# Optimization experiments

Hardware: AMD Instinct MI355X
Metric: run time of the kernel (lower is better)

## Reference

```python
import jax, jax.numpy as jnp
import numpy as np

B, T, C = 2, 2048, 2048
N_HEAD, N_KV_HEAD = 16, 4
HEAD_DIM = C // N_HEAD  # 128
N_REP = N_HEAD // N_KV_HEAD  # 4


def setup_inputs() -> dict:
    key = jax.random.key(0)
    ks = jax.random.split(key, 5)
    x = jax.random.normal(ks[0], (B, T, C), dtype=jnp.float32)
    # RoPE freqs (theta=10000), real cos/sin form of torch's complex freqs_cis
    inv_freq = 1.0 / (10000.0 ** (jnp.arange(0, HEAD_DIM, 2, dtype=jnp.float32) / HEAD_DIM))
    angles = jnp.arange(T, dtype=jnp.float32)[:, None] * inv_freq[None, :]  # [T, HEAD_DIM//2]
    freqs_cos = jnp.cos(angles)
    freqs_sin = jnp.sin(angles)
    s = 0.02
    wq = jax.random.normal(ks[1], (C, C), dtype=jnp.float32) * s
    wk = jax.random.normal(ks[2], (N_KV_HEAD * HEAD_DIM, C), dtype=jnp.float32) * s
    wv = jax.random.normal(ks[3], (N_KV_HEAD * HEAD_DIM, C), dtype=jnp.float32) * s
    wo = jax.random.normal(ks[4], (C, C), dtype=jnp.float32) * s
    return {"x": x, "freqs_cos": freqs_cos, "freqs_sin": freqs_sin,
            "wq": wq, "wk": wk, "wv": wv, "wo": wo}


def _apply_rotary(t, cos, sin):
    # t: [B, T, H, D]; pairs (even, odd) treated as complex, multiplied by cos+i*sin
    tr = t.reshape(*t.shape[:-1], -1, 2)  # [B,T,H,D/2,2]
    t0, t1 = tr[..., 0], tr[..., 1]
    c = cos[None, :, None, :]  # [1,T,1,D/2]
    s = sin[None, :, None, :]
    out = jnp.stack([t0 * c - t1 * s, t0 * s + t1 * c], axis=-1)
    return out.reshape(t.shape)


def reference(x, freqs_cos, freqs_sin, wq, wk, wv, wo):
    b, t, _ = x.shape
    xq = (x @ wq.T).reshape(b, t, N_HEAD, HEAD_DIM)
    xk = (x @ wk.T).reshape(b, t, N_KV_HEAD, HEAD_DIM)
    xv = (x @ wv.T).reshape(b, t, N_KV_HEAD, HEAD_DIM)
    xq = _apply_rotary(xq, freqs_cos, freqs_sin)
    xk = _apply_rotary(xk, freqs_cos, freqs_sin)
    # GQA: repeat_interleave kv heads to n_head
    xk_r = jnp.repeat(xk, N_REP, axis=2)
    xv_r = jnp.repeat(xv, N_REP, axis=2)
    # [B,H,T,D]
    q = xq.transpose(0, 2, 1, 3)
    k = xk_r.transpose(0, 2, 1, 3)
    v = xv_r.transpose(0, 2, 1, 3)
    scale = 1.0 / jnp.sqrt(jnp.float32(HEAD_DIM))
    scores = jnp.einsum('bhtd,bhsd->bhts', q, k) * scale
    causal = jnp.tril(jnp.ones((t, t), dtype=bool))
    scores = jnp.where(causal[None, None], scores, jnp.finfo(scores.dtype).min)
    attn = jax.nn.softmax(scores, axis=-1)
    y = jnp.einsum('bhts,bhsd->bhtd', attn, v)
    y = y.transpose(0, 2, 1, 3).reshape(b, t, C)
    return y @ wo.T
```

## Files before the change

### kernel.cpp

```cpp
#include <hip/hip_runtime.h>

typedef __attribute__((ext_vector_type(8))) __bf16 bf16x8;
typedef __attribute__((ext_vector_type(4))) __bf16 bf16x4;
typedef __attribute__((ext_vector_type(4))) float floatx4;

#define MFMA16x16x32 __builtin_amdgcn_mfma_f32_16x16x32_bf16

__device__ __forceinline__ void async_load16(const void* g, void* l) {
  __builtin_amdgcn_global_load_lds((const __attribute__((address_space(1))) void*)g,
                                   (__attribute__((address_space(3))) void*)l, 16, 0, 0);
}

__global__ __launch_bounds__(256) void cast_all_kernel(const float* __restrict__ x,
                                                       const float* __restrict__ wq,
                                                       const float* __restrict__ wk,
                                                       const float* __restrict__ wv,
                                                       const float* __restrict__ wo,
                                                       __bf16* __restrict__ dst) {
  int i = blockIdx.x * blockDim.x + threadIdx.x;
  const float* src;
  int off;
  if (i < 2097152)      { src = x;  off = 0; }
  else if (i < 3145728) { src = wq; off = 2097152; }
  else if (i < 3407872) { src = wk; off = 3145728; }
  else if (i < 3670016) { src = wv; off = 3407872; }
  else                  { src = wo; off = 3670016; }
  float4 v = ((const float4*)src)[i - off];
  bf16x4 o;
  o[0] = (__bf16)v.x; o[1] = (__bf16)v.y; o[2] = (__bf16)v.z; o[3] = (__bf16)v.w;
  *(bf16x4*)(dst + (size_t)i * 4) = o;
}

template <int MODE>
__global__ __launch_bounds__(256, 3) void gemm_bt(const __bf16* __restrict__ A,
                                                  const __bf16* __restrict__ Bw,
                                                  float* __restrict__ C,
                                                  const float* __restrict__ cs,
                                                  const float* __restrict__ sn,
                                                  __bf16* __restrict__ qb,
                                                  __bf16* __restrict__ kb,
                                                  __bf16* __restrict__ vtg,
                                                  int M, int N, int K) {
  __shared__ __bf16 As[128][64];
  __shared__ __bf16 Bs[128][64];
  const int tid = threadIdx.x;
  const int wave = tid >> 6, lane = tid & 63;
  const int quad = lane >> 4, l16 = lane & 15;
  const int wm = (wave >> 1) * 64, wn = (wave & 1) * 64;
  const int row0 = blockIdx.y * 128, col0 = blockIdx.x * 128;
  const int lr = lane >> 3, ls = lane & 7;
  const int segg = ls ^ lr;
  floatx4 acc[4][4] = {};
  const __bf16* Ab = A + (size_t)row0 * K + segg * 8;
  const __bf16* Bb = Bw + (size_t)col0 * K + segg * 8;
  for (int k0 = 0; k0 < K; k0 += 64) {
    __syncthreads();
#pragma unroll
    for (int i = 0; i < 4; i++) {
      int c = wave * 4 + i;
      int r = c * 8 + lr;
      async_load16(Ab + (size_t)r * K + k0, &As[c * 8][0]);
      async_load16(Bb + (size_t)r * K + k0, &Bs[c * 8][0]);
    }
    __syncthreads();
#pragma unroll
    for (int kk = 0; kk < 64; kk += 32) {
      bf16x8 af[4], bfr[4];
#pragma unroll
      for (int mt = 0; mt < 4; mt++) {
        int row = wm + mt * 16 + l16;
        int seg = ((kk >> 3) + quad) ^ (row & 7);
        af[mt] = *(const bf16x8*)&As[row][seg * 8];
      }
#pragma unroll
      for (int nt = 0; nt < 4; nt++) {
        int row = wn + nt * 16 + l16;
        int seg = ((kk >> 3) + quad) ^ (row & 7);
        bfr[nt] = *(const bf16x8*)&Bs[row][seg * 8];
      }
#pragma unroll
      for (int mt = 0; mt < 4; mt++)
#pragma unroll
        for (int nt = 0; nt < 4; nt++)
          acc[mt][nt] = MFMA16x16x32(af[mt], bfr[nt], acc[mt][nt], 0, 0, 0);
    }
  }
  if (MODE == 0) {
#pragma unroll
    for (int mt = 0; mt < 4; mt++)
#pragma unroll
      for (int nt = 0; nt < 4; nt++)
#pragma unroll
        for (int r = 0; r < 4; r++) {
          int row = row0 + wm + mt * 16 + quad * 4 + r;
          int col = col0 + wn + nt * 16 + l16;
          C[(size_t)row * N + col] = acc[mt][nt][r];
        }
  } else {
#pragma unroll
    for (int mt = 0; mt < 4; mt++)
#pragma unroll
      for (int nt = 0; nt < 4; nt++) {
        const int cbase = col0 + wn + nt * 16;
        if (cbase < 2560) {
          const int c = cbase + l16;
#pragma unroll
          for (int r = 0; r < 4; r++) {
            int row = row0 + wm + mt * 16 + quad * 4 + r;
            int t = row & 2047;
            float v = acc[mt][nt][r];
            float vp = __shfl_xor(v, 1);
            int i = (c & 127) >> 1;
            float co = cs[t * 64 + i], si = sn[t * 64 + i];
            float rv = v * co + ((c & 1) ? vp : -vp) * si;
            if (cbase < 2048) {
              qb[(size_t)row * 2048 + c] = (__bf16)(rv * 0.1275411391f);
            } else {
              kb[(size_t)row * 512 + c - 2048] = (__bf16)rv;
            }
          }
        }
      }
    __syncthreads();
    __bf16* Vl = &As[0][0] + wave * 1024;
    const int brow = row0 + wm;
#pragma unroll
    for (int nt = 0; nt < 4; nt++) {
      const int cbase = col0 + wn + nt * 16;
      if (cbase >= 2560) {
#pragma unroll
        for (int mt = 0; mt < 4; mt++)
#pragma unroll
          for (int r = 0; r < 4; r++)
            Vl[l16 * 64 + mt * 16 + quad * 4 + r] = (__bf16)acc[mt][nt][r];
        asm volatile("" ::: "memory");
        const int vB = cbase - 2560;
#pragma unroll
        for (int p = 0; p < 4; p++) {
          int vdl = p * 4 + (lane >> 4);
          int tl = (lane & 15) * 4;
          bf16x4 val = *(const bf16x4*)&Vl[vdl * 64 + tl];
          *(bf16x4*)&vtg[((size_t)(brow >> 11) * 512 + vB + vdl) * 2048 +
                         (brow & 2047) + tl] = val;
        }
        asm volatile("" ::: "memory");
      }
    }
  }
}

__global__ __launch_bounds__(256, 2) void attn_kernel(const __bf16* __restrict__ qb,
                                                      const __bf16* __restrict__ kb,
                                                      const __bf16* __restrict__ vtg,
                                                      __bf16* __restrict__ yb) {
  const int id = blockIdx.x;
  const int q1 = id >> 8;
  const int cc = id & 255;
  const int kvh = cc & 3;
  const int b = (cc >> 2) & 1;
  const int s5 = (cc >> 3) & 31;
  const int tile = q1 ? (63 - s5) : s5;
  const int tid = threadIdx.x, wave = tid >> 6, lane = tid & 63;
  const int h = kvh * 4 + wave;
  const int quad = lane >> 4, l16 = lane & 15;
  const int q0 = tile * 32;
  __shared__ __bf16 Ks[2][64][128];
  __shared__ __bf16 Vt[2][128][64];
  __shared__ __bf16 Ps[4][2][16][64];
  const __bf16* kbase = kb + (size_t)b * 2048 * 512 + kvh * 128;
  const __bf16* vbase = vtg + ((size_t)b * 512 + kvh * 128) * 2048;

  const int u16   = (quad ^ (l16 & 3)) * 16;
  const int b2_64 = (l16 & 4) ? 64 : 0;
  char* const ksb = (char*)Ks;
  char* const vtb = (char*)Vt;
  char* const psb = (char*)Ps + wave * 4096;
  char* const kA0 = ksb + l16 * 256 + u16 + b2_64;
  char* const kB0 = kA0 + 64 - 2 * b2_64;
  char* const kA1 = kA0 + 16384;
  char* const kB1 = kB0 + 16384;
  char* const vA0 = vtb + l16 * 128 + u16 + b2_64;
  char* const vB0 = vA0 + 64 - 2 * b2_64;
  char* const vA1 = vA0 + 16384;
  char* const vB1 = vB0 + 16384;
  char* const prA = psb + l16 * 128 + u16 + b2_64;
  char* const prB = prA + 64 - 2 * b2_64;
  const int h16 = (l16 & 8) ? 16 : 0;
  const int q64 = (quad & 1) * 64;
  char* const pw00 = psb + quad * 512 + (l16 & 7) * 2 + h16 + q64;
  char* const pw10 = psb + quad * 512 + (l16 & 7) * 2 + (16 - h16) + q64;
  char* const pw01 = pw00 + 64 - 2 * q64;
  char* const pw11 = pw10 + 64 - 2 * q64;

  const int klr4 = lane >> 4, kls = lane & 15;
  const int vlr8 = lane >> 3, vls = lane & 7;
  const __bf16* ksrc[4];
  const __bf16* vsrc[4];
#pragma unroll
  for (int i = 0; i < 4; i++) {
    int row = (wave * 4 + i) * 4 + klr4;
    ksrc[i] = kbase + (size_t)row * 512 + (kls ^ (row & 7)) * 8;
    int d = (wave * 4 + i) * 8 + vlr8;
    vsrc[i] = vbase + (size_t)d * 2048 + (vls ^ (d & 7)) * 8;
  }
  char* const kdst = ksb + wave * 4096;
  char* const vdst = vtb + wave * 4096;

  auto stage = [&](int pb, int s0) {
#pragma unroll
    for (int i = 0; i < 4; i++)
      async_load16(ksrc[i] + (size_t)s0 * 512, kdst + pb * 16384 + i * 1024);
#pragma unroll
    for (int i = 0; i < 4; i++)
      async_load16(vsrc[i] + s0, vdst + pb * 16384 + i * 1024);
  };

  bf16x8 qf[2][4];
#pragma unroll
  for (int mt = 0; mt < 2; mt++)
#pragma unroll
    for (int kc = 0; kc < 4; kc++)
      qf[mt][kc] = *(const bf16x8*)(qb + (size_t)(b * 2048 + q0 + mt * 16 + l16) * 2048 +
                                    h * 128 + kc * 32 + quad * 8);
  bf16x8 ones;
#pragma unroll
  for (int j = 0; j < 8; j++) ones[j] = (__bf16)1.0f;
  floatx4 o[2][8] = {};
  floatx4 lsum[2] = {};
  const int nblocks = (tile + 2) >> 1;

  stage(0, 0);

  for (int it = 0; it < nblocks; it++) {
    const int cur = it & 1;
    const int s0 = it * 64;
    asm volatile("s_barrier" ::: "memory");
    if (it + 1 < nblocks) {
      stage(cur ^ 1, s0 + 64);
      asm volatile("s_waitcnt vmcnt(8)" ::: "memory");
    } else {
      asm volatile("s_waitcnt vmcnt(0)" ::: "memory");
    }
    asm volatile("s_barrier" ::: "memory");
    const char* kA = cur ? kA1 : kA0;
    const char* kB = cur ? kB1 : kB0;
    const char* vA = cur ? vA1 : vA0;
    const char* vB = cur ? vB1 : vB0;
    floatx4 sacc[2][4] = {};
    __builtin_amdgcn_s_setprio(1);
#pragma unroll
    for (int kc = 0; kc < 4; kc++) {
      const char* kbp = (kc & 1) ? kB : kA;
      bf16x8 bfr[4];
#pragma unroll
      for (int nt = 0; nt < 4; nt++)
        bfr[nt] = *(const bf16x8*)(kbp + nt * 4096 + (kc >> 1) * 128);
#pragma unroll
      for (int mt = 0; mt < 2; mt++)
#pragma unroll
        for (int nt = 0; nt < 4; nt++)
          sacc[mt][nt] = MFMA16x16x32(qf[mt][kc], bfr[nt], sacc[mt][nt], 0, 0, 0);
    }
    __builtin_amdgcn_s_setprio(0);
    const bool diag = (it == nblocks - 1);
#pragma unroll
    for (int mt = 0; mt < 2; mt++)
#pragma unroll
      for (int r = 0; r < 4; r++) {
        const int qg = q0 + mt * 16 + quad * 4 + r;
#pragma unroll
        for (int nt = 0; nt < 4; nt++) {
          float p = __builtin_exp2f(sacc[mt][nt][r]);
          if (diag) { int keyg = s0 + nt * 16 + l16; p = (keyg <= qg) ? p : 0.f; }
          char* w = (r & 1) ? ((nt < 2) ? pw10 : pw11) : ((nt < 2) ? pw00 : pw01);
          *(__bf16*)(w + mt * 2048 + r * 128 + ((nt & 1) ^ (r >> 1)) * 32) = (__bf16)p;
        }
      }
    __builtin_amdgcn_s_setprio(1);
#pragma unroll
    for (int c2 = 0; c2 < 2; c2++) {
      const char* pr = c2 ? prB : prA;
      const char* vv = c2 ? vB : vA;
      bf16x8 pa[2];
#pragma unroll
      for (int mt = 0; mt < 2; mt++) {
        pa[mt] = *(const bf16x8*)(pr + mt * 2048);
        lsum[mt] = MFMA16x16x32(pa[mt], ones, lsum[mt], 0, 0, 0);
      }
#pragma unroll
      for (int dt = 0; dt < 8; dt++) {
        bf16x8 vf = *(const bf16x8*)(vv + dt * 2048);
#pragma unroll
        for (int mt = 0; mt < 2; mt++)
          o[mt][dt] = MFMA16x16x32(pa[mt], vf, o[mt][dt], 0, 0, 0);
      }
    }
    __builtin_amdgcn_s_setprio(0);
  }
#pragma unroll
  for (int mt = 0; mt < 2; mt++) {
    float inv[4];
#pragma unroll
    for (int r = 0; r < 4; r++) inv[r] = 1.f / lsum[mt][r];
#pragma unroll
    for (int dt = 0; dt < 8; dt++)
#pragma unroll
      for (int r = 0; r < 4; r++) {
        int qg = q0 + mt * 16 + quad * 4 + r;
        yb[(size_t)(b * 2048 + qg) * 2048 + h * 128 + dt * 16 + l16] =
            (__bf16)(o[mt][dt][r] * inv[r]);
      }
  }
}

extern "C" void kernel_launch(void* const* d_in, const int* in_sizes, int n_in,
                              void* d_out, int out_size, void* d_ws, size_t ws_size,
                              hipStream_t stream) {
  const float* x  = (const float*)d_in[0];
  const float* fc = (const float*)d_in[1];
  const float* fs = (const float*)d_in[2];
  const float* wq = (const float*)d_in[3];
  const float* wk = (const float*)d_in[4];
  const float* wv = (const float*)d_in[5];
  const float* wo = (const float*)d_in[6];
  float* out = (float*)d_out;
  char* ws = (char*)d_ws;

  __bf16* xb   = (__bf16*)(ws);
  __bf16* wqkv = (__bf16*)(ws + 16777216);
  __bf16* wob  = (__bf16*)(ws + 29360128);
  __bf16* qbuf = (__bf16*)(ws + 37748736);
  __bf16* kbuf = (__bf16*)(ws + 54525952);
  __bf16* vtg  = (__bf16*)(ws + 58720256);
  __bf16* ybuf = (__bf16*)(ws + 62914560);

  cast_all_kernel<<<18432, 256, 0, stream>>>(x, wq, wk, wv, wo, xb);

  gemm_bt<1><<<dim3(24, 32), 256, 0, stream>>>(xb, wqkv, nullptr, fc, fs,
                                               qbuf, kbuf, vtg, 4096, 3072, 2048);

  attn_kernel<<<dim3(512), 256, 0, stream>>>(qbuf, kbuf, vtg, ybuf);

  gemm_bt<0><<<dim3(16, 32), 256, 0, stream>>>(ybuf, wob, out, nullptr, nullptr,
                                               nullptr, nullptr, nullptr, 4096, 2048, 2048);
}
```

Baseline: 307.6 us.

## Split attention key range across two wave groups with LDS reduction

```diff
diff --git a/kernel.cpp b/kernel.cpp
--- a/kernel.cpp
+++ b/kernel.cpp
@@ -149,167 +149,194 @@
   }
 }
 
-__global__ __launch_bounds__(256, 2) void attn_kernel(const __bf16* __restrict__ qb,
+__global__ __launch_bounds__(512, 4) void attn_kernel(const __bf16* __restrict__ qb,
                                                       const __bf16* __restrict__ kb,
                                                       const __bf16* __restrict__ vtg,
                                                       __bf16* __restrict__ yb) {
   const int id = blockIdx.x;
-  const int q1 = id >> 8;
-  const int cc = id & 255;
-  const int kvh = cc & 3;
-  const int b = (cc >> 2) & 1;
-  const int s5 = (cc >> 3) & 31;
-  const int tile = q1 ? (63 - s5) : s5;
+  const int kvh = id & 3, b = (id >> 2) & 1;
+  const int tile = id >> 3;
   const int tid = threadIdx.x, wave = tid >> 6, lane = tid & 63;
-  const int h = kvh * 4 + wave;
+  const int ck = wave >> 2, hw = wave & 3;
+  const int h = kvh * 4 + hw;
   const int quad = lane >> 4, l16 = lane & 15;
   const int q0 = tile * 32;
-  __shared__ __bf16 Ks[2][64][128];
+  const int nk = tile + 1;
+  const int c0 = nk >> 1;
+  const int L = nk - c0;
+
+  __shared__ __bf16 Ks[2][2][32][128];
   __shared__ __bf16 Vt[2][128][64];
-  __shared__ __bf16 Ps[4][2][16][64];
+  __shared__ __bf16 Ps[8][2][16][32];
+
   const __bf16* kbase = kb + (size_t)b * 2048 * 512 + kvh * 128;
   const __bf16* vbase = vtg + ((size_t)b * 512 + kvh * 128) * 2048;
 
-  const int u16   = (quad ^ (l16 & 3)) * 16;
+  const int kl = lane >> 4, ks16 = lane & 15;
+  const __bf16* ksrc[2]; char* kdst[2];
+#pragma unroll
+  for (int jj = 0; jj < 2; jj++) {
+    int krow = hw * 8 + jj * 4 + kl;
+    ksrc[jj] = kbase + (size_t)krow * 512 + (ks16 ^ (krow & 7)) * 8;
+    kdst[jj] = (char*)Ks + ck * 8192 + (hw * 8 + jj * 4) * 256;
+  }
+  const int vdl = lane >> 2, vks = lane & 3;
+  const __bf16* vsrc[2]; char* vdst[2];
+#pragma unroll
+  for (int jj = 0; jj < 2; jj++) {
+    int d = hw * 32 + jj * 16 + vdl;
+    vsrc[jj] = vbase + (size_t)d * 2048 + vks * 8;
+    vdst[jj] = (char*)Vt + d * 128 + (((ck * 4 + vks) ^ (d & 7)) * 16);
+  }
+
+  const int u16 = (quad ^ (l16 & 3)) * 16;
   const int b2_64 = (l16 & 4) ? 64 : 0;
-  char* const ksb = (char*)Ks;
-  char* const vtb = (char*)Vt;
-  char* const psb = (char*)Ps + wave * 4096;
-  char* const kA0 = ksb + l16 * 256 + u16 + b2_64;
+  char* const kA0 = (char*)Ks + ck * 8192 + l16 * 256 + u16 + b2_64;
   char* const kB0 = kA0 + 64 - 2 * b2_64;
-  char* const kA1 = kA0 + 16384;
-  char* const kB1 = kB0 + 16384;
-  char* const vA0 = vtb + l16 * 128 + u16 + b2_64;
-  char* const vB0 = vA0 + 64 - 2 * b2_64;
-  char* const vA1 = vA0 + 16384;
-  char* const vB1 = vB0 + 16384;
-  char* const prA = psb + l16 * 128 + u16 + b2_64;
-  char* const prB = prA + 64 - 2 * b2_64;
-  const int h16 = (l16 & 8) ? 16 : 0;
-  const int q64 = (quad & 1) * 64;
-  char* const pw00 = psb + quad * 512 + (l16 & 7) * 2 + h16 + q64;
-  char* const pw10 = psb + quad * 512 + (l16 & 7) * 2 + (16 - h16) + q64;
-  char* const pw01 = pw00 + 64 - 2 * q64;
-  char* const pw11 = pw10 + 64 - 2 * q64;
-
-  const int klr4 = lane >> 4, kls = lane & 15;
-  const int vlr8 = lane >> 3, vls = lane & 7;
-  const __bf16* ksrc[4];
-  const __bf16* vsrc[4];
-#pragma unroll
-  for (int i = 0; i < 4; i++) {
-    int row = (wave * 4 + i) * 4 + klr4;
-    ksrc[i] = kbase + (size_t)row * 512 + (kls ^ (row & 7)) * 8;
-    int d = (wave * 4 + i) * 8 + vlr8;
-    vsrc[i] = vbase + (size_t)d * 2048 + (vls ^ (d & 7)) * 8;
-  }
-  char* const kdst = ksb + wave * 4096;
-  char* const vdst = vtb + wave * 4096;
-
-  auto stage = [&](int pb, int s0) {
-#pragma unroll
-    for (int i = 0; i < 4; i++)
-      async_load16(ksrc[i] + (size_t)s0 * 512, kdst + pb * 16384 + i * 1024);
-#pragma unroll
-    for (int i = 0; i < 4; i++)
-      async_load16(vsrc[i] + s0, vdst + pb * 16384 + i * 1024);
-  };
-
-  bf16x8 qf[2][4];
-#pragma unroll
-  for (int mt = 0; mt < 2; mt++)
-#pragma unroll
-    for (int kc = 0; kc < 4; kc++)
-      qf[mt][kc] = *(const bf16x8*)(qb + (size_t)(b * 2048 + q0 + mt * 16 + l16) * 2048 +
-                                    h * 128 + kc * 32 + quad * 8);
+  char* const vrd0 = (char*)Vt + l16 * 128 + u16 + ((ck ^ ((l16 >> 2) & 1)) ? 64 : 0);
+  char* const psb = (char*)Ps + wave * 2048;
+  char* const prd = psb + l16 * 64 + u16;
+  const int h3 = (l16 >> 3) & 1;
+  char* const pwE = psb + quad * 256 + (l16 & 7) * 2 + h3 * 16;
+  char* const pwO = psb + quad * 256 + (l16 & 7) * 2 + 16 - h3 * 16;
+
   bf16x8 ones;
 #pragma unroll
   for (int j = 0; j < 8; j++) ones[j] = (__bf16)1.0f;
   floatx4 o[2][8] = {};
   floatx4 lsum[2] = {};
-  const int nblocks = (tile + 2) >> 1;
-
-  stage(0, 0);
-
-  for (int it = 0; it < nblocks; it++) {
-    const int cur = it & 1;
-    const int s0 = it * 64;
+
+  {
+    const int g0 = ck ? c0 : 0;
+    bf16x8 v0 = *(const bf16x8*)(vsrc[0] + g0 * 32);
+    bf16x8 v1 = *(const bf16x8*)(vsrc[1] + g0 * 32);
+#pragma unroll
+    for (int jj = 0; jj < 2; jj++)
+      async_load16(ksrc[jj] + (size_t)g0 * 16384, kdst[jj]);
+    *(bf16x8*)(vdst[0]) = v0;
+    *(bf16x8*)(vdst[1]) = v1;
+  }
+
+  for (int it = 0; it < L; it++) {
+    const int cur = it & 1, nxt = cur ^ 1;
+    const int cu16 = cur << 14;
+    asm volatile("s_waitcnt lgkmcnt(0)" ::: "memory");
     asm volatile("s_barrier" ::: "memory");
-    if (it + 1 < nblocks) {
-      stage(cur ^ 1, s0 + 64);
-      asm volatile("s_waitcnt vmcnt(8)" ::: "memory");
+    const bool pf = (it + 1 < L);
+    int gn = 0;
+    if (pf) {
+      gn = ck ? (c0 + it + 1) : min(it + 1, c0 > 0 ? c0 - 1 : 0);
+#pragma unroll
+      for (int jj = 0; jj < 2; jj++)
+        async_load16(ksrc[jj] + (size_t)gn * 16384, kdst[jj] + nxt * 16384);
+      asm volatile("s_waitcnt vmcnt(2)" ::: "memory");
     } else {
       asm volatile("s_waitcnt vmcnt(0)" ::: "memory");
     }
     asm volatile("s_barrier" ::: "memory");
-    const char* kA = cur ? kA1 : kA0;
-    const char* kB = cur ? kB1 : kB0;
-    const char* vA = cur ? vA1 : vA0;
-    const char* vB = cur ? vB1 : vB0;
-    floatx4 sacc[2][4] = {};
+
+    floatx4 sacc[2][2] = {};
+    const char* kA = kA0 + cu16;
+    const char* kB = kB0 + cu16;
     __builtin_amdgcn_s_setprio(1);
 #pragma unroll
     for (int kc = 0; kc < 4; kc++) {
-      const char* kbp = (kc & 1) ? kB : kA;
-      bf16x8 bfr[4];
-#pragma unroll
-      for (int nt = 0; nt < 4; nt++)
-        bfr[nt] = *(const bf16x8*)(kbp + nt * 4096 + (kc >> 1) * 128);
+      bf16x8 qfr[2];
 #pragma unroll
       for (int mt = 0; mt < 2; mt++)
-#pragma unroll
-        for (int nt = 0; nt < 4; nt++)
-          sacc[mt][nt] = MFMA16x16x32(qf[mt][kc], bfr[nt], sacc[mt][nt], 0, 0, 0);
+        qfr[mt] = *(const bf16x8*)(qb + (size_t)(b * 2048 + q0 + mt * 16 + l16) * 2048 +
+                                   h * 128 + kc * 32 + quad * 8);
+      const char* kp = (kc & 1) ? kB : kA;
+      bf16x8 bf0 = *(const bf16x8*)(kp + (kc >> 1) * 128);
+      bf16x8 bf1 = *(const bf16x8*)(kp + 4096 + (kc >> 1) * 128);
+#pragma unroll
+      for (int mt = 0; mt < 2; mt++) {
+        sacc[mt][0] = MFMA16x16x32(qfr[mt], bf0, sacc[mt][0], 0, 0, 0);
+        sacc[mt][1] = MFMA16x16x32(qfr[mt], bf1, sacc[mt][1], 0, 0, 0);
+      }
     }
     __builtin_amdgcn_s_setprio(0);
-    const bool diag = (it == nblocks - 1);
+
+    bf16x8 vr0, vr1;
+    if (pf) {
+      vr0 = *(const bf16x8*)(vsrc[0] + gn * 32);
+      vr1 = *(const bf16x8*)(vsrc[1] + gn * 32);
+    }
+
+    const int gq = ck ? (c0 + it) : it;
+    const bool diag = (ck == 1) && (it == L - 1);
+    const bool inval = (ck == 0) && (it >= c0);
 #pragma unroll
     for (int mt = 0; mt < 2; mt++)
 #pragma unroll
       for (int r = 0; r < 4; r++) {
         const int qg = q0 + mt * 16 + quad * 4 + r;
 #pragma unroll
-        for (int nt = 0; nt < 4; nt++) {
+        for (int nt = 0; nt < 2; nt++) {
           float p = __builtin_exp2f(sacc[mt][nt][r]);
-          if (diag) { int keyg = s0 + nt * 16 + l16; p = (keyg <= qg) ? p : 0.f; }
-          char* w = (r & 1) ? ((nt < 2) ? pw10 : pw11) : ((nt < 2) ? pw00 : pw01);
-          *(__bf16*)(w + mt * 2048 + r * 128 + ((nt & 1) ^ (r >> 1)) * 32) = (__bf16)p;
-        }
-      }
+          if (diag) { int keyg = gq * 32 + nt * 16 + l16; p = (keyg <= qg) ? p : 0.f; }
+          if (inval) p = 0.f;
+          char* w = (r & 1) ? pwO : pwE;
+          *(__bf16*)(w + mt * 1024 + r * 64 + ((nt ^ ((r >> 1) & 1)) * 32)) = (__bf16)p;
+        }
+      }
+
     __builtin_amdgcn_s_setprio(1);
-#pragma unroll
-    for (int c2 = 0; c2 < 2; c2++) {
-      const char* pr = c2 ? prB : prA;
-      const char* vv = c2 ? vB : vA;
-      bf16x8 pa[2];
+    bf16x8 pa[2];
+#pragma unroll
+    for (int mt = 0; mt < 2; mt++) {
+      pa[mt] = *(const bf16x8*)(prd + mt * 1024);
+      lsum[mt] = MFMA16x16x32(pa[mt], ones, lsum[mt], 0, 0, 0);
+    }
+    const char* vv = vrd0 + cu16;
+#pragma unroll
+    for (int dt = 0; dt < 8; dt++) {
+      bf16x8 vf = *(const bf16x8*)(vv + dt * 2048);
+      o[0][dt] = MFMA16x16x32(pa[0], vf, o[0][dt], 0, 0, 0);
+      o[1][dt] = MFMA16x16x32(pa[1], vf, o[1][dt], 0, 0, 0);
+    }
+    __builtin_amdgcn_s_setprio(0);
+
+    if (pf) {
+      *(bf16x8*)(vdst[0] + nxt * 16384) = vr0;
+      *(bf16x8*)(vdst[1] + nxt * 16384) = vr1;
+    }
+  }
+
+  asm volatile("s_barrier" ::: "memory");
+  {
+    char* mo = (hw < 2) ? ((char*)Ks + hw * 16384) : ((char*)Vt + (hw - 2) * 16384);
+    char* ml = (char*)Ps + (4 + hw) * 2048;
+    if (ck == 1) {
 #pragma unroll
       for (int mt = 0; mt < 2; mt++) {
-        pa[mt] = *(const bf16x8*)(pr + mt * 2048);
-        lsum[mt] = MFMA16x16x32(pa[mt], ones, lsum[mt], 0, 0, 0);
-      }
-#pragma unroll
-      for (int dt = 0; dt < 8; dt++) {
-        bf16x8 vf = *(const bf16x8*)(vv + dt * 2048);
-#pragma unroll
-        for (int mt = 0; mt < 2; mt++)
-          o[mt][dt] = MFMA16x16x32(pa[mt], vf, o[mt][dt], 0, 0, 0);
-      }
-    }
-    __builtin_amdgcn_s_setprio(0);
-  }
-#pragma unroll
-  for (int mt = 0; mt < 2; mt++) {
-    float inv[4];
-#pragma unroll
-    for (int r = 0; r < 4; r++) inv[r] = 1.f / lsum[mt][r];
-#pragma unroll
-    for (int dt = 0; dt < 8; dt++)
-#pragma unroll
-      for (int r = 0; r < 4; r++) {
-        int qg = q0 + mt * 16 + quad * 4 + r;
-        yb[(size_t)(b * 2048 + qg) * 2048 + h * 128 + dt * 16 + l16] =
-            (__bf16)(o[mt][dt][r] * inv[r]);
-      }
+#pragma unroll
+        for (int dt = 0; dt < 8; dt++)
+          *(floatx4*)(mo + ((mt * 8 + dt) * 64 + lane) * 16) = o[mt][dt];
+        *(floatx4*)(ml + (mt * 64 + lane) * 16) = lsum[mt];
+      }
+    }
+    asm volatile("s_waitcnt lgkmcnt(0)" ::: "memory");
+    asm volatile("s_barrier" ::: "memory");
+    if (ck == 0) {
+#pragma unroll
+      for (int mt = 0; mt < 2; mt++) {
+        lsum[mt] += *(const floatx4*)(ml + (mt * 64 + lane) * 16);
+        float inv[4];
+#pragma unroll
+        for (int r = 0; r < 4; r++) inv[r] = 1.f / lsum[mt][r];
+#pragma unroll
+        for (int dt = 0; dt < 8; dt++) {
+          floatx4 op = *(const floatx4*)(mo + ((mt * 8 + dt) * 64 + lane) * 16);
+#pragma unroll
+          for (int r = 0; r < 4; r++) {
+            int qg = q0 + mt * 16 + quad * 4 + r;
+            yb[(size_t)(b * 2048 + qg) * 2048 + h * 128 + dt * 16 + l16] =
+                (__bf16)((o[mt][dt][r] + op[r]) * inv[r]);
+          }
+        }
+      }
+    }
   }
 }
 
@@ -339,7 +366,7 @@
   gemm_bt<1><<<dim3(24, 32), 256, 0, stream>>>(xb, wqkv, nullptr, fc, fs,
                                                qbuf, kbuf, vtg, 4096, 3072, 2048);
 
-  attn_kernel<<<dim3(512), 256, 0, stream>>>(qbuf, kbuf, vtg, ybuf);
+  attn_kernel<<<dim3(512), 512, 0, stream>>>(qbuf, kbuf, vtg, ybuf);
 
   gemm_bt<0><<<dim3(16, 32), 256, 0, stream>>>(ybuf, wob, out, nullptr, nullptr,
                                                nullptr, nullptr, nullptr, 4096, 2048, 2048);
```

Result: slower. 424.5 us (+38.0%).

## Restructure GEMMs into 256-row tiles with double-buffered async LDS pipeline

Applied to the files above, without the earlier changes.

```diff
diff --git a/kernel.cpp b/kernel.cpp
--- a/kernel.cpp
+++ b/kernel.cpp
@@ -31,8 +31,8 @@
   *(bf16x4*)(dst + (size_t)i * 4) = o;
 }
 
-template <int MODE>
-__global__ __launch_bounds__(256, 3) void gemm_bt(const __bf16* __restrict__ A,
+template <int MODE, int BN>
+__global__ __launch_bounds__(512, 1) void gemm_bt(const __bf16* __restrict__ A,
                                                   const __bf16* __restrict__ Bw,
                                                   float* __restrict__ C,
                                                   const float* __restrict__ cs,
@@ -41,72 +41,107 @@
                                                   __bf16* __restrict__ kb,
                                                   __bf16* __restrict__ vtg,
                                                   int M, int N, int K) {
-  __shared__ __bf16 As[128][64];
-  __shared__ __bf16 Bs[128][64];
+  constexpr int NW = BN / 4;
+  constexpr int NF = NW / 16;
+  constexpr int NBI = BN / 64;
+  __shared__ __bf16 As[2][256][64];
+  __shared__ __bf16 Bs[2][BN][64];
   const int tid = threadIdx.x;
   const int wave = tid >> 6, lane = tid & 63;
   const int quad = lane >> 4, l16 = lane & 15;
-  const int wm = (wave >> 1) * 64, wn = (wave & 1) * 64;
-  const int row0 = blockIdx.y * 128, col0 = blockIdx.x * 128;
+  const int wm2 = wave >> 2, wn4 = wave & 3;
   const int lr = lane >> 3, ls = lane & 7;
   const int segg = ls ^ lr;
-  floatx4 acc[4][4] = {};
+
+  const int nwg = gridDim.x;
+  const int wg = (blockIdx.x & 7) * (nwg >> 3) + (blockIdx.x >> 3);
+  const int GY = M >> 8;
+  const int by = wg % GY, bx = wg / GY;
+  const int row0 = by * 256, col0 = bx * BN;
+
+  floatx4 acc[8][NF] = {};
   const __bf16* Ab = A + (size_t)row0 * K + segg * 8;
   const __bf16* Bb = Bw + (size_t)col0 * K + segg * 8;
-  for (int k0 = 0; k0 < K; k0 += 64) {
-    __syncthreads();
-#pragma unroll
-    for (int i = 0; i < 4; i++) {
-      int c = wave * 4 + i;
-      int r = c * 8 + lr;
-      async_load16(Ab + (size_t)r * K + k0, &As[c * 8][0]);
-      async_load16(Bb + (size_t)r * K + k0, &Bs[c * 8][0]);
-    }
-    __syncthreads();
-#pragma unroll
-    for (int kk = 0; kk < 64; kk += 32) {
-      bf16x8 af[4], bfr[4];
-#pragma unroll
-      for (int mt = 0; mt < 4; mt++) {
-        int row = wm + mt * 16 + l16;
-        int seg = ((kk >> 3) + quad) ^ (row & 7);
-        af[mt] = *(const bf16x8*)&As[row][seg * 8];
-      }
-#pragma unroll
-      for (int nt = 0; nt < 4; nt++) {
-        int row = wn + nt * 16 + l16;
-        int seg = ((kk >> 3) + quad) ^ (row & 7);
-        bfr[nt] = *(const bf16x8*)&Bs[row][seg * 8];
-      }
-#pragma unroll
-      for (int mt = 0; mt < 4; mt++)
-#pragma unroll
-        for (int nt = 0; nt < 4; nt++)
-          acc[mt][nt] = MFMA16x16x32(af[mt], bfr[nt], acc[mt][nt], 0, 0, 0);
-    }
-  }
+
+  auto stage = [&](int sb, int k0) {
+#pragma unroll
+    for (int i = 0; i < 4; i++)
+      async_load16(Ab + (size_t)(wave * 32 + i * 8 + lr) * K + k0,
+                   &As[sb][wave * 32 + i * 8][0]);
+#pragma unroll
+    for (int j = 0; j < NBI; j++)
+      async_load16(Bb + (size_t)(wave * (BN / 8) + j * 8 + lr) * K + k0,
+                   &Bs[sb][wave * (BN / 8) + j * 8][0]);
+  };
+
+  const int NS = K >> 6;
+  stage(0, 0);
+  stage(1, 64);
+
+#pragma unroll 2
+  for (int s = 0; s < NS; s++) {
+    const int c = s & 1;
+    if (s == NS - 1) {
+      asm volatile("s_waitcnt vmcnt(0)" ::: "memory");
+    } else if constexpr (NBI == 3) {
+      asm volatile("s_waitcnt vmcnt(7)" ::: "memory");
+    } else {
+      asm volatile("s_waitcnt vmcnt(6)" ::: "memory");
+    }
+    __builtin_amdgcn_s_barrier();
+
+    bf16x8 af[2][8], bfr[2][NF];
+#pragma unroll
+    for (int kk = 0; kk < 2; kk++) {
+#pragma unroll
+      for (int mt = 0; mt < 8; mt++) {
+        int row = wm2 * 128 + mt * 16 + l16;
+        int seg = (kk * 4 + quad) ^ (row & 7);
+        af[kk][mt] = *(const bf16x8*)&As[c][row][seg * 8];
+      }
+#pragma unroll
+      for (int nt = 0; nt < NF; nt++) {
+        int row = wn4 * NW + nt * 16 + l16;
+        int seg = (kk * 4 + quad) ^ (row & 7);
+        bfr[kk][nt] = *(const bf16x8*)&Bs[c][row][seg * 8];
+      }
+    }
+    asm volatile("s_waitcnt lgkmcnt(0)" ::: "memory");
+    __builtin_amdgcn_s_barrier();
+    if (s + 2 < NS) stage(c, (s + 2) * 64);
+    __builtin_amdgcn_s_setprio(1);
+#pragma unroll
+    for (int kk = 0; kk < 2; kk++)
+#pragma unroll
+      for (int mt = 0; mt < 8; mt++)
+#pragma unroll
+        for (int nt = 0; nt < NF; nt++)
+          acc[mt][nt] = MFMA16x16x32(af[kk][mt], bfr[kk][nt], acc[mt][nt], 0, 0, 0);
+    __builtin_amdgcn_s_setprio(0);
+  }
+
   if (MODE == 0) {
 #pragma unroll
-    for (int mt = 0; mt < 4; mt++)
-#pragma unroll
-      for (int nt = 0; nt < 4; nt++)
+    for (int mt = 0; mt < 8; mt++)
+#pragma unroll
+      for (int nt = 0; nt < NF; nt++)
 #pragma unroll
         for (int r = 0; r < 4; r++) {
-          int row = row0 + wm + mt * 16 + quad * 4 + r;
-          int col = col0 + wn + nt * 16 + l16;
+          int row = row0 + wm2 * 128 + mt * 16 + quad * 4 + r;
+          int col = col0 + wn4 * NW + nt * 16 + l16;
           C[(size_t)row * N + col] = acc[mt][nt][r];
         }
   } else {
 #pragma unroll
-    for (int mt = 0; mt < 4; mt++)
-#pragma unroll
-      for (int nt = 0; nt < 4; nt++) {
-        const int cbase = col0 + wn + nt * 16;
+    for (int mt = 0; mt < 8; mt++)
+#pragma unroll
+      for (int nt = 0; nt < NF; nt++) {
+        const int cbase = col0 + wn4 * NW + nt * 16;
         if (cbase < 2560) {
           const int c = cbase + l16;
 #pragma unroll
           for (int r = 0; r < 4; r++) {
-            int row = row0 + wm + mt * 16 + quad * 4 + r;
+            int row = row0 + wm2 * 128 + mt * 16 + quad * 4 + r;
             int t = row & 2047;
             float v = acc[mt][nt][r];
             float vp = __shfl_xor(v, 1);
@@ -121,27 +156,26 @@
           }
         }
       }
-    __syncthreads();
-    __bf16* Vl = &As[0][0] + wave * 1024;
-    const int brow = row0 + wm;
-#pragma unroll
-    for (int nt = 0; nt < 4; nt++) {
-      const int cbase = col0 + wn + nt * 16;
+    __bf16* Vl = &As[0][0][0] + wave * 2048;
+    const int brow = row0 + wm2 * 128;
+    const int bb = brow >> 11, trow = brow & 2047;
+#pragma unroll
+    for (int nt = 0; nt < NF; nt++) {
+      const int cbase = col0 + wn4 * NW + nt * 16;
       if (cbase >= 2560) {
 #pragma unroll
-        for (int mt = 0; mt < 4; mt++)
+        for (int mt = 0; mt < 8; mt++)
 #pragma unroll
           for (int r = 0; r < 4; r++)
-            Vl[l16 * 64 + mt * 16 + quad * 4 + r] = (__bf16)acc[mt][nt][r];
+            Vl[l16 * 128 + mt * 16 + quad * 4 + r] = (__bf16)acc[mt][nt][r];
         asm volatile("" ::: "memory");
         const int vB = cbase - 2560;
 #pragma unroll
         for (int p = 0; p < 4; p++) {
-          int vdl = p * 4 + (lane >> 4);
-          int tl = (lane & 15) * 4;
-          bf16x4 val = *(const bf16x4*)&Vl[vdl * 64 + tl];
-          *(bf16x4*)&vtg[((size_t)(brow >> 11) * 512 + vB + vdl) * 2048 +
-                         (brow & 2047) + tl] = val;
+          int vd = p * 4 + (lane >> 4);
+          int t0 = (lane & 15) * 8;
+          bf16x8 val = *(const bf16x8*)&Vl[vd * 128 + t0];
+          *(bf16x8*)&vtg[((size_t)bb * 512 + vB + vd) * 2048 + trow + t0] = val;
         }
         asm volatile("" ::: "memory");
       }
@@ -336,11 +370,11 @@
 
   cast_all_kernel<<<18432, 256, 0, stream>>>(x, wq, wk, wv, wo, xb);
 
-  gemm_bt<1><<<dim3(24, 32), 256, 0, stream>>>(xb, wqkv, nullptr, fc, fs,
-                                               qbuf, kbuf, vtg, 4096, 3072, 2048);
-
-  attn_kernel<<<dim3(512), 256, 0, stream>>>(qbuf, kbuf, vtg, ybuf);
-
-  gemm_bt<0><<<dim3(16, 32), 256, 0, stream>>>(ybuf, wob, out, nullptr, nullptr,
-                                               nullptr, nullptr, nullptr, 4096, 2048, 2048);
-}
+  gemm_bt<1, 192><<<256, 512, 0, stream>>>(xb, wqkv, nullptr, fc, fs,
+                                           qbuf, kbuf, vtg, 4096, 3072, 2048);
+
+  attn_kernel<<<512, 256, 0, stream>>>(qbuf, kbuf, vtg, ybuf);
+
+  gemm_bt<0, 128><<<256, 512, 0, stream>>>(ybuf, wob, out, nullptr, nullptr,
+                                           nullptr, nullptr, nullptr, 4096, 2048, 2048);
+}
```

Result: no change. 304.3 us (-1.1%).
